# Kernel tuning notes

Measured on AMD Instinct MI355X. Metric: run time of the kernel, lower is better.

The kernel has to match this reference:

```python
import jax, jax.numpy as jnp
import numpy as np

N_NODES = 100000
IN_FEAT = 128
HIDDEN = 256
OUT = 2
N_EDGES = 600000
EPS = 1e-12  # F.normalize eps


def glorot(key, shape):
    fan_in, fan_out = shape[1], shape[0]
    lim = jnp.sqrt(6.0 / (fan_in + fan_out))
    return jax.random.uniform(key, shape, jnp.float32, -lim, lim)


def setup_inputs() -> dict:
    key = jax.random.key(0)
    ks = jax.random.split(key, 8)
    x = jax.random.normal(ks[0], (N_NODES, IN_FEAT), jnp.float32)
    edge_index = jax.random.randint(ks[1], (2, N_EDGES), 0, N_NODES, jnp.int64)
    return {
        'x': x,
        'edge_index': edge_index,
        'W1_l': glorot(ks[2], (HIDDEN, IN_FEAT)),
        'b1': jnp.zeros((HIDDEN,), jnp.float32),
        'W1_r': glorot(ks[3], (HIDDEN, IN_FEAT)),
        'W2_l': glorot(ks[4], (OUT, HIDDEN)),
        'b2': jnp.zeros((OUT,), jnp.float32),
        'W2_r': glorot(ks[5], (OUT, HIDDEN)),
    }


def sage_conv(x, src, dst, W_l, b_l, W_r):
    # mean aggregation of neighbor (source) features onto destination nodes
    msgs = x[src]  # [E, d]
    s = jax.ops.segment_sum(msgs, dst, num_segments=N_NODES)
    cnt = jax.ops.segment_sum(jnp.ones((src.shape[0], 1), x.dtype), dst,
                              num_segments=N_NODES)
    agg = s / jnp.maximum(cnt, 1.0)  # nodes with no in-edges stay 0
    out = agg @ W_l.T + b_l + x @ W_r.T  # lin_l(agg) + lin_r(x)
    # L2 normalize (normalize=True in SAGEConv)
    nrm = jnp.linalg.norm(out, axis=-1, keepdims=True)
    return out / jnp.maximum(nrm, EPS)


def reference(x, edge_index, W1_l, b1, W1_r, W2_l, b2, W2_r):
    src, dst = edge_index[0], edge_index[1]
    h = sage_conv(x, src, dst, W1_l, b1, W1_r)
    h = jax.nn.relu(h)
    # dropout(p=0.2) is identity in eval mode
    h = sage_conv(h, src, dst, W2_l, b2, W2_r)
    return jax.nn.log_softmax(h, axis=1)
```

## Files before the change

kernel.cpp:

```cpp
#include <hip/hip_runtime.h>
#include <hip/hip_fp16.h>

#define NN  100000
#define FIN 128
#define HID 256
#define NE  600000
#define FEPS 1e-12f


typedef _Float16 f16x8 __attribute__((ext_vector_type(8)));
typedef float    f32x4 __attribute__((ext_vector_type(4)));

__device__ __forceinline__ int clampN(int v) {
    return ((unsigned)v < (unsigned)NN) ? v : 0;
}
__device__ __forceinline__ int detect4(const int* ei) {
    return ((ei[1] | ei[3] | ei[5] | ei[7]) == 0) ? 1 : 0;
}
__device__ __forceinline__ int ld_src(const int* ei, int e, int f) {
    return f ? ei[2 * e] : ei[e];
}
__device__ __forceinline__ int ld_dst(const int* ei, int e, int f) {
    return f ? ei[2 * (NE + e)] : ei[NE + e];
}

__device__ __forceinline__ unsigned packh2(__half a, __half b) {
    return __builtin_bit_cast(unsigned, __halves2half2(a, b));
}

__device__ __forceinline__ size_t fragIdx(int j, int k) {
    return ((size_t)((k >> 5) * 16 + (j >> 4)) * 64 +
            (size_t)(((k >> 3) & 3) * 16 + (j & 15))) * 8 + (k & 7);
}

__global__ __launch_bounds__(256) void setup_kernel(
    const int* __restrict__ ei,
    const float* __restrict__ x,
    const float* __restrict__ W1l, const float* __restrict__ W1r,
    __half* __restrict__ Bfh, __half* __restrict__ Bfl,
    __half* __restrict__ xh,
    int* __restrict__ cnt, int ncv)
{
    int b = blockIdx.x;
    int t = threadIdx.x;
    if (b < 256) {
        int j = b, k2 = t;
        float v = (k2 < FIN) ? W1l[(size_t)j * FIN + k2]
                             : W1r[(size_t)j * FIN + (k2 - FIN)];
        __half h  = __float2half_rn(v);
        __half lo = __float2half_rn(v - __half2float(h));
        size_t fi = fragIdx(j, k2);
        Bfh[fi] = h;
        Bfl[fi] = lo;
    } else if (b < 256 + ncv) {
        int idx = (b - 256) * 256 + t;
        if (idx < NN * FIN / 8) {
            const float4* px = (const float4*)(x + (size_t)idx * 8);
            float4 v0 = px[0], v1 = px[1];
            uint4 u;
            u.x = packh2(__float2half_rn(v0.x), __float2half_rn(v0.y));
            u.y = packh2(__float2half_rn(v0.z), __float2half_rn(v0.w));
            u.z = packh2(__float2half_rn(v1.x), __float2half_rn(v1.y));
            u.w = packh2(__float2half_rn(v1.z), __float2half_rn(v1.w));
            ((uint4*)xh)[idx] = u;
        }
    } else {
        int e = (b - 256 - ncv) * 256 + t;
        if (e < NE) {
            int f = detect4(ei);
            atomicAdd(cnt + clampN(ld_dst(ei, e, f)), 1);
        }
    }
}

__global__ __launch_bounds__(1024) void scan_a_kernel(
    const int* __restrict__ cnt, int* __restrict__ off, int* __restrict__ bsum)
{
    __shared__ int sm[1024];
    int t = threadIdx.x;
    int idx = blockIdx.x * 1024 + t;
    int v = (idx < NN) ? cnt[idx] : 0;
    sm[t] = v;
    __syncthreads();
    for (int d = 1; d < 1024; d <<= 1) {
        int w = (t >= d) ? sm[t - d] : 0;
        __syncthreads();
        sm[t] += w;
        __syncthreads();
    }
    if (idx < NN) off[idx] = sm[t] - v;
    if (t == 1023) bsum[blockIdx.x] = sm[1023];
}
__global__ __launch_bounds__(128) void scan_b_kernel(
    int* __restrict__ bsum, int* __restrict__ off, int nblocks)
{
    __shared__ int sm[128];
    int t = threadIdx.x;
    int v = (t < nblocks) ? bsum[t] : 0;
    sm[t] = v;
    __syncthreads();
    for (int d = 1; d < 128; d <<= 1) {
        int w = (t >= d) ? sm[t - d] : 0;
        __syncthreads();
        sm[t] += w;
        __syncthreads();
    }
    if (t < nblocks) bsum[t] = sm[t] - v;
    if (t == 0) off[NN] = NE;
}
__global__ __launch_bounds__(1024) void scan_c_kernel(
    const int* __restrict__ bsum, int* __restrict__ off)
{
    int idx = blockIdx.x * 1024 + threadIdx.x;
    if (idx < NN) off[idx] += bsum[blockIdx.x];
}

__global__ __launch_bounds__(256) void fill_kernel(
    const int* __restrict__ ei,
    const int* __restrict__ off, int* __restrict__ cur, int* __restrict__ col)
{
    int e = blockIdx.x * 256 + threadIdx.x;
    if (e >= NE) return;
    int f = detect4(ei);
    int src = clampN(ld_src(ei, e, f));
    int dst = clampN(ld_dst(ei, e, f));
    int p = atomicAdd(cur + dst, 1);
    col[off[dst] + p] = src;
}

__global__ __launch_bounds__(256) void gather_kernel(
    const int* __restrict__ off, const int* __restrict__ col,
    const __half* __restrict__ xh,
    __half* __restrict__ aggH, __half* __restrict__ aggL)
{
    int idx = blockIdx.x * 256 + threadIdx.x;
    if (idx >= NN * 16) return;
    int n     = idx >> 4;
    int ft    = idx & 15;
    int fbase = ft * 8;

    float a[8];
#pragma unroll
    for (int i = 0; i < 8; ++i) a[i] = 0.0f;

    int s0 = off[n], s1 = off[n + 1];
    int i = s0;
    for (; i + 3 < s1; i += 4) {
        int c0 = clampN(col[i]);
        int c1 = clampN(col[i + 1]);
        int c2 = clampN(col[i + 2]);
        int c3 = clampN(col[i + 3]);
        uint4 v0 = *(const uint4*)(xh + (size_t)c0 * FIN + fbase);
        uint4 v1 = *(const uint4*)(xh + (size_t)c1 * FIN + fbase);
        uint4 v2 = *(const uint4*)(xh + (size_t)c2 * FIN + fbase);
        uint4 v3 = *(const uint4*)(xh + (size_t)c3 * FIN + fbase);
#pragma unroll
        for (int u = 0; u < 4; ++u) {
            float2 f0 = __half22float2(__builtin_bit_cast(__half2, (&v0.x)[u]));
            float2 f1 = __half22float2(__builtin_bit_cast(__half2, (&v1.x)[u]));
            float2 f2 = __half22float2(__builtin_bit_cast(__half2, (&v2.x)[u]));
            float2 f3 = __half22float2(__builtin_bit_cast(__half2, (&v3.x)[u]));
            a[2 * u]     += (f0.x + f1.x) + (f2.x + f3.x);
            a[2 * u + 1] += (f0.y + f1.y) + (f2.y + f3.y);
        }
    }
    for (; i < s1; ++i) {
        int c0 = clampN(col[i]);
        uint4 v0 = *(const uint4*)(xh + (size_t)c0 * FIN + fbase);
#pragma unroll
        for (int u = 0; u < 4; ++u) {
            float2 f0 = __half22float2(__builtin_bit_cast(__half2, (&v0.x)[u]));
            a[2 * u]     += f0.x;
            a[2 * u + 1] += f0.y;
        }
    }
    float ic = 1.0f / fmaxf((float)(s1 - s0), 1.0f);
    __half h[8], lo[8];
#pragma unroll
    for (int k = 0; k < 8; ++k) {
        float v = a[k] * ic;
        h[k]  = __float2half_rn(v);
        lo[k] = __float2half_rn(v - __half2float(h[k]));
    }
    uint4 uh, ul;
    uh.x = packh2(h[0], h[1]);  uh.y = packh2(h[2], h[3]);
    uh.z = packh2(h[4], h[5]);  uh.w = packh2(h[6], h[7]);
    ul.x = packh2(lo[0], lo[1]); ul.y = packh2(lo[2], lo[3]);
    ul.z = packh2(lo[4], lo[5]); ul.w = packh2(lo[6], lo[7]);
    size_t rowb = (size_t)n * 128 + (size_t)((ft ^ (n & 7)) << 3);
    *(uint4*)(aggH + rowb) = uh;
    *(uint4*)(aggL + rowb) = ul;
}

__device__ __forceinline__ void splitStore4(
    __half* Ah, __half* Al, int addr, float4 v)
{
    __half h0 = __float2half_rn(v.x), h1 = __float2half_rn(v.y);
    __half h2 = __float2half_rn(v.z), h3 = __float2half_rn(v.w);
    __half l0 = __float2half_rn(v.x - __half2float(h0));
    __half l1 = __float2half_rn(v.y - __half2float(h1));
    __half l2 = __float2half_rn(v.z - __half2float(h2));
    __half l3 = __float2half_rn(v.w - __half2float(h3));
    uint2 uh, ul;
    uh.x = packh2(h0, h1);  uh.y = packh2(h2, h3);
    ul.x = packh2(l0, l1);  ul.y = packh2(l2, l3);
    *(uint2*)(Ah + addr) = uh;
    *(uint2*)(Al + addr) = ul;
}

__device__ __forceinline__ void mfma_phase(
    const __half* Ah, const __half* Al,
    const __half* __restrict__ Bfh, const __half* __restrict__ Bfl,
    int pb , int baseA0, int baseA1, int r7,
    int jg0, int l, f32x4 acc[2][4])
{
    const int kg = l >> 4;
#pragma unroll
    for (int kk = 0; kk < 4; ++kk) {
        const int chunk = kk * 4 + kg;
        const int sl = (chunk ^ r7) << 3;
        f16x8 ah0 = *reinterpret_cast<const f16x8*>(Ah + baseA0 + sl);
        f16x8 al0 = *reinterpret_cast<const f16x8*>(Al + baseA0 + sl);
        f16x8 ah1 = *reinterpret_cast<const f16x8*>(Ah + baseA1 + sl);
        f16x8 al1 = *reinterpret_cast<const f16x8*>(Al + baseA1 + sl);
#pragma unroll
        for (int jt = 0; jt < 4; ++jt) {
            const size_t bo = (((size_t)(pb + kk) * 16 + jg0 + jt) * 64 + l) * 8;
            f16x8 bh = *reinterpret_cast<const f16x8*>(Bfh + bo);
            f16x8 bl = *reinterpret_cast<const f16x8*>(Bfl + bo);
            acc[0][jt] = __builtin_amdgcn_mfma_f32_16x16x32_f16(ah0, bh, acc[0][jt], 0, 0, 0);
            acc[1][jt] = __builtin_amdgcn_mfma_f32_16x16x32_f16(ah1, bh, acc[1][jt], 0, 0, 0);
            acc[0][jt] = __builtin_amdgcn_mfma_f32_16x16x32_f16(al0, bh, acc[0][jt], 0, 0, 0);
            acc[1][jt] = __builtin_amdgcn_mfma_f32_16x16x32_f16(al1, bh, acc[1][jt], 0, 0, 0);
            acc[0][jt] = __builtin_amdgcn_mfma_f32_16x16x32_f16(ah0, bl, acc[0][jt], 0, 0, 0);
            acc[1][jt] = __builtin_amdgcn_mfma_f32_16x16x32_f16(ah1, bl, acc[1][jt], 0, 0, 0);
        }
    }
}

__global__ __launch_bounds__(512, 4) void gemm_mfma_kernel(
    const __half* __restrict__ aggH, const __half* __restrict__ aggL,
    const float* __restrict__ x,
    const __half* __restrict__ Bfh, const __half* __restrict__ Bfl,
    const float* __restrict__ b1,
    const float* __restrict__ W2l, const float* __restrict__ W2r,
    float* __restrict__ g, float* __restrict__ r)
{
    __shared__ __half Ah[64 * 128];
    __shared__ __half Al[64 * 128];

    const int t  = threadIdx.x;
    const int nb = blockIdx.x * 64;

    {
        const uint4* gh = (const uint4*)(aggH + (size_t)nb * 128);
        const uint4* gl = (const uint4*)(aggL + (size_t)nb * 128);
#pragma unroll
        for (int i = 0; i < 2; ++i) {
            int idx = i * 512 + t;
            *(uint4*)(Ah + idx * 8) = gh[idx];
            *(uint4*)(Al + idx * 8) = gl[idx];
        }
    }
    __syncthreads();

    const int l     = t & 63;
    const int w     = t >> 6;
    const int ln    = l & 15;
    const int kg    = l >> 4;
    const int mrow0 = (w & 1) * 32;
    const int jg0   = (w >> 1) * 4;

    f32x4 acc[2][4];
#pragma unroll
    for (int mt = 0; mt < 2; ++mt)
#pragma unroll
        for (int jt = 0; jt < 4; ++jt)
            acc[mt][jt] = (f32x4){0.f, 0.f, 0.f, 0.f};

    const int rowA0  = mrow0 + ln;
    const int rowA1  = mrow0 + 16 + ln;
    const int baseA0 = rowA0 * 128;
    const int baseA1 = rowA1 * 128;
    const int r7     = ln & 7;

    mfma_phase(Ah, Al, Bfh, Bfl, 0, baseA0, baseA1, r7, jg0, l, acc);
    __syncthreads();

    {
        const float4* xF = (const float4*)x;
        const float4 z4 = make_float4(0.f, 0.f, 0.f, 0.f);
#pragma unroll
        for (int i = 0; i < 4; ++i) {
            int idx   = i * 512 + t;
            int n_loc = idx >> 5;
            int kq    = idx & 31;
            int n     = nb + n_loc;
            float4 v  = (n < NN) ? xF[(size_t)n * 32 + kq] : z4;
            int addr  = n_loc * 128 + ((((kq >> 1) ^ (n_loc & 7)) << 3) | ((kq & 1) << 2));
            splitStore4(Ah, Al, addr, v);
        }
    }
    __syncthreads();

    mfma_phase(Ah, Al, Bfh, Bfl, 4, baseA0, baseA1, r7, jg0, l, acc);

    const int jb2 = jg0 * 16;
    float b1v[4], wl0[4], wl1[4], wr0[4], wr1[4];
#pragma unroll
    for (int jt = 0; jt < 4; ++jt) {
        int j = jb2 + jt * 16 + ln;
        b1v[jt] = b1[j];
        wl0[jt] = W2l[j];        wl1[jt] = W2l[HID + j];
        wr0[jt] = W2r[j];        wr1[jt] = W2r[HID + j];
    }

    __syncthreads();
    float* red = (float*)Ah;
#pragma unroll
    for (int mt = 0; mt < 2; ++mt) {
#pragma unroll
        for (int rg = 0; rg < 4; ++rg) {
            float s = 0.f, G0 = 0.f, G1 = 0.f, R0 = 0.f, R1 = 0.f;
#pragma unroll
            for (int jt = 0; jt < 4; ++jt) {
                float oo = acc[mt][jt][rg] + b1v[jt];
                s = fmaf(oo, oo, s);
                float pp = fmaxf(oo, 0.f);
                G0 = fmaf(pp, wl0[jt], G0);
                G1 = fmaf(pp, wl1[jt], G1);
                R0 = fmaf(pp, wr0[jt], R0);
                R1 = fmaf(pp, wr1[jt], R1);
            }
#pragma unroll
            for (int m = 1; m < 16; m <<= 1) {
                s  += __shfl_xor(s, m);
                G0 += __shfl_xor(G0, m);
                G1 += __shfl_xor(G1, m);
                R0 += __shfl_xor(R0, m);
                R1 += __shfl_xor(R1, m);
            }
            if (ln == 0) {
                int n_loc = mrow0 + mt * 16 + kg * 4 + rg;
                float* pp = red + ((size_t)(w >> 1) * 64 + n_loc) * 5;
                pp[0] = s;  pp[1] = G0; pp[2] = G1; pp[3] = R0; pp[4] = R1;
            }
        }
    }
    __syncthreads();

    if (t < 64) {
        int n = nb + t;
        if (n < NN) {
            float s = 0.f, G0 = 0.f, G1 = 0.f, R0 = 0.f, R1 = 0.f;
#pragma unroll
            for (int jg = 0; jg < 4; ++jg) {
                const float* pp = red + ((size_t)jg * 64 + t) * 5;
                s += pp[0]; G0 += pp[1]; G1 += pp[2]; R0 += pp[3]; R1 += pp[4];
            }
            float inv = 1.0f / fmaxf(sqrtf(s), FEPS);
            g[2 * (size_t)n]     = G0 * inv;
            g[2 * (size_t)n + 1] = G1 * inv;
            r[2 * (size_t)n]     = R0 * inv;
            r[2 * (size_t)n + 1] = R1 * inv;
        }
    }
}

__device__ __forceinline__ void phaseB_epilogue(
    float* smem_f, int t, int l, int nb,
    const __half* __restrict__ Bfh, const __half* __restrict__ Bfl,
    const float* __restrict__ b1,
    const float* __restrict__ W2l, const float* __restrict__ W2r,
    float* __restrict__ g, float* __restrict__ r)
{
    const int w  = __builtin_amdgcn_readfirstlane(t >> 6);
    const int jb = w * 16;

    float o[16];
#pragma unroll
    for (int i = 0; i < 16; ++i) o[i] = 0.0f;

#pragma unroll 1
    for (int k2 = 0; k2 < 2 * FIN; k2 += 4) {
        const int nc = l ^ ((k2 >> 3) & 31);
        float av0 = smem_f[(k2 + 0) * 64 + nc];
        float av1 = smem_f[(k2 + 1) * 64 + nc];
        float av2 = smem_f[(k2 + 2) * 64 + nc];
        float av3 = smem_f[(k2 + 3) * 64 + nc];
#pragma unroll
        for (int i = 0; i < 16; ++i) {
            const size_t fb = ((size_t)((k2 >> 5) * 16 + ((jb + i) >> 4)) * 64 +
                               (size_t)(((k2 >> 3) & 3) * 16 + ((jb + i) & 15))) * 8 +
                              (k2 & 7);
            const __half* ph = Bfh + fb;
            const __half* pl = Bfl + fb;
            float oi = o[i];
            oi = fmaf(av0, __half2float(ph[0]) + __half2float(pl[0]), oi);
            oi = fmaf(av1, __half2float(ph[1]) + __half2float(pl[1]), oi);
            oi = fmaf(av2, __half2float(ph[2]) + __half2float(pl[2]), oi);
            oi = fmaf(av3, __half2float(ph[3]) + __half2float(pl[3]), oi);
            o[i] = oi;
        }
    }

    float sq = 0.f, g0 = 0.f, g1 = 0.f, r0 = 0.f, r1 = 0.f;
    const float* b1w  = b1  + jb;
    const float* w2la = W2l + jb;
    const float* w2lb = W2l + HID + jb;
    const float* w2ra = W2r + jb;
    const float* w2rb = W2r + HID + jb;
#pragma unroll
    for (int i = 0; i < 16; ++i) {
        float oo = o[i] + b1w[i];
        sq = fmaf(oo, oo, sq);
        float p = fmaxf(oo, 0.0f);
        g0 = fmaf(p, w2la[i], g0);
        g1 = fmaf(p, w2lb[i], g1);
        r0 = fmaf(p, w2ra[i], r0);
        r1 = fmaf(p, w2rb[i], r1);
    }

    __syncthreads();
    smem_f[0 * 1024 + t] = sq;
    smem_f[1 * 1024 + t] = g0;
    smem_f[2 * 1024 + t] = g1;
    smem_f[3 * 1024 + t] = r0;
    smem_f[4 * 1024 + t] = r1;
    __syncthreads();

    if (t < 64) {
        int n2 = nb + t;
        float sqs = 0.f, G0 = 0.f, G1 = 0.f, R0 = 0.f, R1 = 0.f;
#pragma unroll
        for (int ww = 0; ww < 16; ++ww) {
            sqs += smem_f[0 * 1024 + ww * 64 + t];
            G0  += smem_f[1 * 1024 + ww * 64 + t];
            G1  += smem_f[2 * 1024 + ww * 64 + t];
            R0  += smem_f[3 * 1024 + ww * 64 + t];
            R1  += smem_f[4 * 1024 + ww * 64 + t];
        }
        float inv = 1.0f / fmaxf(sqrtf(sqs), FEPS);
        if (n2 < NN) {
            g[2 * (size_t)n2]     = G0 * inv;
            g[2 * (size_t)n2 + 1] = G1 * inv;
            r[2 * (size_t)n2]     = R0 * inv;
            r[2 * (size_t)n2 + 1] = R1 * inv;
        }
    }
}

template <bool HALFX>
__global__ __launch_bounds__(1024, 8) void layer1_kernel(
    const int* __restrict__ off, const int* __restrict__ col,
    const float* __restrict__ x, const __half* __restrict__ xh,
    const __half* __restrict__ Bfh, const __half* __restrict__ Bfl,
    const float* __restrict__ b1,
    const float* __restrict__ W2l, const float* __restrict__ W2r,
    float* __restrict__ g, float* __restrict__ r)
{
    __shared__ float smem_f[256 * 64];

    const int t  = threadIdx.x;
    const int nb = blockIdx.x * 64;
    const int l  = t & 63;

    {
        const int n_loc = t >> 4;
        const int ft    = t & 15;
        const int fbase = ft * 8;
        const int n     = nb + n_loc;
        const bool valid = (n < NN);

        float a[8];
#pragma unroll
        for (int i = 0; i < 8; ++i) a[i] = 0.0f;

        int s0 = 0, s1 = 0;
        if (valid) { s0 = off[n]; s1 = off[n + 1]; }

        int i = s0;
        if (HALFX) {
            for (; i + 3 < s1; i += 4) {
                int c0 = clampN(col[i]);
                int c1 = clampN(col[i + 1]);
                int c2 = clampN(col[i + 2]);
                int c3 = clampN(col[i + 3]);
                uint4 v0 = *(const uint4*)(xh + (size_t)c0 * FIN + fbase);
                uint4 v1 = *(const uint4*)(xh + (size_t)c1 * FIN + fbase);
                uint4 v2 = *(const uint4*)(xh + (size_t)c2 * FIN + fbase);
                uint4 v3 = *(const uint4*)(xh + (size_t)c3 * FIN + fbase);
#pragma unroll
                for (int u = 0; u < 4; ++u) {
                    float2 f0 = __half22float2(__builtin_bit_cast(__half2, (&v0.x)[u]));
                    float2 f1 = __half22float2(__builtin_bit_cast(__half2, (&v1.x)[u]));
                    float2 f2 = __half22float2(__builtin_bit_cast(__half2, (&v2.x)[u]));
                    float2 f3 = __half22float2(__builtin_bit_cast(__half2, (&v3.x)[u]));
                    a[2 * u]     += (f0.x + f1.x) + (f2.x + f3.x);
                    a[2 * u + 1] += (f0.y + f1.y) + (f2.y + f3.y);
                }
            }
            for (; i < s1; ++i) {
                int c0 = clampN(col[i]);
                uint4 v0 = *(const uint4*)(xh + (size_t)c0 * FIN + fbase);
#pragma unroll
                for (int u = 0; u < 4; ++u) {
                    float2 f0 = __half22float2(__builtin_bit_cast(__half2, (&v0.x)[u]));
                    a[2 * u]     += f0.x;
                    a[2 * u + 1] += f0.y;
                }
            }
        } else {
            for (; i < s1; ++i) {
                int c0 = clampN(col[i]);
                const float4* p0 = (const float4*)(x + (size_t)c0 * FIN + fbase);
                float4 v00 = p0[0], v01 = p0[1];
                a[0] += v00.x; a[1] += v00.y; a[2] += v00.z; a[3] += v00.w;
                a[4] += v01.x; a[5] += v01.y; a[6] += v01.z; a[7] += v01.w;
            }
        }
        float ic = 1.0f / fmaxf((float)(s1 - s0), 1.0f);
#pragma unroll
        for (int k = 0; k < 8; ++k) {
            int f = fbase + k;
            smem_f[f * 64 + (n_loc ^ ((f >> 3) & 31))] = a[k] * ic;
        }
        const float4* sp = (const float4*)(x + (size_t)(valid ? n : 0) * FIN + fbase);
        float4 s0v = valid ? sp[0] : make_float4(0.f, 0.f, 0.f, 0.f);
        float4 s1v = valid ? sp[1] : make_float4(0.f, 0.f, 0.f, 0.f);
        float sv[8] = {s0v.x, s0v.y, s0v.z, s0v.w, s1v.x, s1v.y, s1v.z, s1v.w};
#pragma unroll
        for (int k = 0; k < 8; ++k) {
            int f = FIN + fbase + k;
            smem_f[f * 64 + (n_loc ^ ((f >> 3) & 31))] = sv[k];
        }
    }
    __syncthreads();

    phaseB_epilogue(smem_f, t, l, nb, Bfh, Bfl, b1, W2l, W2r, g, r);
}

__global__ __launch_bounds__(256) void finalize_kernel(
    const int* __restrict__ off, const int* __restrict__ col,
    const float* __restrict__ g, const float* __restrict__ r,
    const float* __restrict__ b2,
    float* __restrict__ out)
{
    int n = blockIdx.x * 256 + threadIdx.x;
    if (n >= NN) return;
    int s0 = off[n], s1 = off[n + 1];
    float z0 = 0.0f, z1 = 0.0f, y0b = 0.0f, y1b = 0.0f;
    int i = s0;
    for (; i + 1 < s1; i += 2) {
        int sa = clampN(col[i]);
        int sb = clampN(col[i + 1]);
        float2 va = *(const float2*)(g + 2 * (size_t)sa);
        float2 vb = *(const float2*)(g + 2 * (size_t)sb);
        z0 += va.x; z1 += va.y;
        y0b += vb.x; y1b += vb.y;
    }
    if (i < s1) {
        int sa = clampN(col[i]);
        float2 va = *(const float2*)(g + 2 * (size_t)sa);
        z0 += va.x; z1 += va.y;
    }
    z0 += y0b; z1 += y1b;
    float ic = 1.0f / fmaxf((float)(s1 - s0), 1.0f);
    z0 = z0 * ic + b2[0] + r[2 * (size_t)n];
    z1 = z1 * ic + b2[1] + r[2 * (size_t)n + 1];
    float d = 1.0f / fmaxf(sqrtf(z0 * z0 + z1 * z1), FEPS);
    float y0 = z0 * d, y1 = z1 * d;
    float m = fmaxf(y0, y1);
    float lg = m + logf(__expf(y0 - m) + __expf(y1 - m));
    out[2 * (size_t)n]     = y0 - lg;
    out[2 * (size_t)n + 1] = y1 - lg;
}

extern "C" void kernel_launch(void* const* d_in, const int* in_sizes, int n_in,
                              void* d_out, int out_size, void* d_ws, size_t ws_size,
                              hipStream_t stream) {
    const float* x   = (const float*)d_in[0];
    const int*   ei  = (const int*)d_in[1];
    const float* W1l = (const float*)d_in[2];
    const float* b1  = (const float*)d_in[3];
    const float* W1r = (const float*)d_in[4];
    const float* W2l = (const float*)d_in[5];
    const float* b2  = (const float*)d_in[6];
    const float* W2r = (const float*)d_in[7];

    const int nsb = (NN + 1023) / 1024;
    const int ncv = (NN * FIN / 8 + 255) / 256;
    const int ecb = (NE + 255) / 256;

    const size_t tailWords = (size_t)2 * NN + (NN + 1) + NE + 4 * NN + 128;
    const size_t needB = (size_t)256 * 256 * 4 + (size_t)NN * FIN * 2 +
                         tailWords * 4;
    const size_t needA = needB + (size_t)NN * FIN * 4;

    bool pathA = (ws_size >= needA);
    bool pathB = !pathA && (ws_size >= needB);
    bool half  = pathA || pathB;

    char* p = (char*)d_ws;
    __half* Bfh = (__half*)p;             p += (size_t)256 * 256 * 2;
    __half* Bfl = (__half*)p;             p += (size_t)256 * 256 * 2;
    __half* xh = nullptr;
    if (half) { xh = (__half*)p;          p += (size_t)NN * FIN * 2; }
    __half* aggH = nullptr; __half* aggL = nullptr;
    if (pathA) {
        aggH = (__half*)p;
        aggL = aggH + (size_t)NN * 128;
        p += (size_t)NN * FIN * 4;
    }

    int*   cnt  = (int*)p;
    int*   cur  = cnt + NN;
    int*   off  = cur + NN;
    int*   col  = off + NN + 1;
    float* g    = (float*)(col + NE);
    float* r    = g + 2 * (size_t)NN;
    int*   bsum = (int*)(r + 2 * (size_t)NN);

    hipMemsetAsync(cnt, 0, 2 * (size_t)NN * sizeof(int), stream);

    int cv = half ? ncv : 0;
    setup_kernel<<<256 + cv + ecb, 256, 0, stream>>>(ei, x, W1l, W1r,
                                                     Bfh, Bfl, xh, cnt, cv);
    scan_a_kernel<<<nsb, 1024, 0, stream>>>(cnt, off, bsum);
    scan_b_kernel<<<1, 128, 0, stream>>>(bsum, off, nsb);
    scan_c_kernel<<<nsb, 1024, 0, stream>>>(bsum, off);
    fill_kernel<<<ecb, 256, 0, stream>>>(ei, off, cur, col);

    if (pathA) {
        gather_kernel<<<(NN * 16 + 255) / 256, 256, 0, stream>>>(off, col, xh,
                                                                 aggH, aggL);
        gemm_mfma_kernel<<<(NN + 63) / 64, 512, 0, stream>>>(aggH, aggL, x,
                                                             Bfh, Bfl,
                                                             b1, W2l, W2r, g, r);
    } else if (pathB) {
        layer1_kernel<true><<<(NN + 63) / 64, 1024, 0, stream>>>(
            off, col, x, xh, Bfh, Bfl, b1, W2l, W2r, g, r);
    } else {
        layer1_kernel<false><<<(NN + 63) / 64, 1024, 0, stream>>>(
            off, col, x, xh, Bfh, Bfl, b1, W2l, W2r, g, r);
    }
    finalize_kernel<<<(NN + 255) / 256, 256, 0, stream>>>(off, col, g, r, b2,
                                                          (float*)d_out);
}
```

Baseline: 271.2 us.

## Enlarge GEMM tile to 128 rows so each wave reuses B fragments across 8 row tiles

The layer-1 MFMA GEMM kernel now processes 128 nodes per block instead of 64, and each wave covers all 8 row tiles for 2 column groups instead of 2 row tiles for 4 column groups. B fragments from global memory are loaded once per k-step and reused across the 8 row tiles, which cuts global B traffic per node in half. In exchange, A reads from LDS rise, LDS use doubles to 64KB per block (lowering occupancy), and the grid is halved. The change also zero-pads aggregated rows past NN and adds a no-op line in an unrelated epilogue.

```diff
diff --git a/kernel.cpp b/kernel.cpp
--- a/kernel.cpp
+++ b/kernel.cpp
@@ -211,29 +211,30 @@
 __device__ __forceinline__ void mfma_phase(
     const __half* Ah, const __half* Al,
     const __half* __restrict__ Bfh, const __half* __restrict__ Bfl,
-    int pb , int baseA0, int baseA1, int r7,
-    int jg0, int l, f32x4 acc[2][4])
-{
-    const int kg = l >> 4;
+    int pb , int ln, int kg, int r7,
+    int jg0, int l, f32x4 acc[8][2])
+{
 #pragma unroll
     for (int kk = 0; kk < 4; ++kk) {
         const int chunk = kk * 4 + kg;
         const int sl = (chunk ^ r7) << 3;
-        f16x8 ah0 = *reinterpret_cast<const f16x8*>(Ah + baseA0 + sl);
-        f16x8 al0 = *reinterpret_cast<const f16x8*>(Al + baseA0 + sl);
-        f16x8 ah1 = *reinterpret_cast<const f16x8*>(Ah + baseA1 + sl);
-        f16x8 al1 = *reinterpret_cast<const f16x8*>(Al + baseA1 + sl);
-#pragma unroll
-        for (int jt = 0; jt < 4; ++jt) {
-            const size_t bo = (((size_t)(pb + kk) * 16 + jg0 + jt) * 64 + l) * 8;
-            f16x8 bh = *reinterpret_cast<const f16x8*>(Bfh + bo);
-            f16x8 bl = *reinterpret_cast<const f16x8*>(Bfl + bo);
-            acc[0][jt] = __builtin_amdgcn_mfma_f32_16x16x32_f16(ah0, bh, acc[0][jt], 0, 0, 0);
-            acc[1][jt] = __builtin_amdgcn_mfma_f32_16x16x32_f16(ah1, bh, acc[1][jt], 0, 0, 0);
-            acc[0][jt] = __builtin_amdgcn_mfma_f32_16x16x32_f16(al0, bh, acc[0][jt], 0, 0, 0);
-            acc[1][jt] = __builtin_amdgcn_mfma_f32_16x16x32_f16(al1, bh, acc[1][jt], 0, 0, 0);
-            acc[0][jt] = __builtin_amdgcn_mfma_f32_16x16x32_f16(ah0, bl, acc[0][jt], 0, 0, 0);
-            acc[1][jt] = __builtin_amdgcn_mfma_f32_16x16x32_f16(ah1, bl, acc[1][jt], 0, 0, 0);
+        const size_t bo0 = (((size_t)(pb + kk) * 16 + jg0 + 0) * 64 + l) * 8;
+        const size_t bo1 = (((size_t)(pb + kk) * 16 + jg0 + 1) * 64 + l) * 8;
+        f16x8 bh0 = *reinterpret_cast<const f16x8*>(Bfh + bo0);
+        f16x8 bl0 = *reinterpret_cast<const f16x8*>(Bfl + bo0);
+        f16x8 bh1 = *reinterpret_cast<const f16x8*>(Bfh + bo1);
+        f16x8 bl1 = *reinterpret_cast<const f16x8*>(Bfl + bo1);
+#pragma unroll
+        for (int mt = 0; mt < 8; ++mt) {
+            const int base = (mt * 16 + ln) * 128 + sl;
+            f16x8 ah = *reinterpret_cast<const f16x8*>(Ah + base);
+            f16x8 al = *reinterpret_cast<const f16x8*>(Al + base);
+            acc[mt][0] = __builtin_amdgcn_mfma_f32_16x16x32_f16(ah, bh0, acc[mt][0], 0, 0, 0);
+            acc[mt][1] = __builtin_amdgcn_mfma_f32_16x16x32_f16(ah, bh1, acc[mt][1], 0, 0, 0);
+            acc[mt][0] = __builtin_amdgcn_mfma_f32_16x16x32_f16(al, bh0, acc[mt][0], 0, 0, 0);
+            acc[mt][1] = __builtin_amdgcn_mfma_f32_16x16x32_f16(al, bh1, acc[mt][1], 0, 0, 0);
+            acc[mt][0] = __builtin_amdgcn_mfma_f32_16x16x32_f16(ah, bl0, acc[mt][0], 0, 0, 0);
+            acc[mt][1] = __builtin_amdgcn_mfma_f32_16x16x32_f16(ah, bl1, acc[mt][1], 0, 0, 0);
         }
     }
 }
@@ -246,20 +247,24 @@
     const float* __restrict__ W2l, const float* __restrict__ W2r,
     float* __restrict__ g, float* __restrict__ r)
 {
-    __shared__ __half Ah[64 * 128];
-    __shared__ __half Al[64 * 128];
+    __shared__ __half Ah[128 * 128];
+    __shared__ __half Al[128 * 128];
 
     const int t  = threadIdx.x;
-    const int nb = blockIdx.x * 64;
+    const int nb = blockIdx.x * 128;
 
     {
         const uint4* gh = (const uint4*)(aggH + (size_t)nb * 128);
         const uint4* gl = (const uint4*)(aggL + (size_t)nb * 128);
-#pragma unroll
-        for (int i = 0; i < 2; ++i) {
+        const uint4 z4 = make_uint4(0u, 0u, 0u, 0u);
+#pragma unroll
+        for (int i = 0; i < 4; ++i) {
             int idx = i * 512 + t;
-            *(uint4*)(Ah + idx * 8) = gh[idx];
-            *(uint4*)(Al + idx * 8) = gl[idx];
+            bool valid = (nb + (idx >> 4)) < NN;
+            uint4 vh = valid ? gh[idx] : z4;
+            uint4 vl = valid ? gl[idx] : z4;
+            *(uint4*)(Ah + idx * 8) = vh;
+            *(uint4*)(Al + idx * 8) = vl;
         }
     }
     __syncthreads();
@@ -268,30 +273,24 @@
     const int w     = t >> 6;
     const int ln    = l & 15;
     const int kg    = l >> 4;
-    const int mrow0 = (w & 1) * 32;
-    const int jg0   = (w >> 1) * 4;
-
-    f32x4 acc[2][4];
-#pragma unroll
-    for (int mt = 0; mt < 2; ++mt)
-#pragma unroll
-        for (int jt = 0; jt < 4; ++jt)
-            acc[mt][jt] = (f32x4){0.f, 0.f, 0.f, 0.f};
-
-    const int rowA0  = mrow0 + ln;
-    const int rowA1  = mrow0 + 16 + ln;
-    const int baseA0 = rowA0 * 128;
-    const int baseA1 = rowA1 * 128;
-    const int r7     = ln & 7;
-
-    mfma_phase(Ah, Al, Bfh, Bfl, 0, baseA0, baseA1, r7, jg0, l, acc);
+    const int jg0   = w * 2;
+    const int r7    = ln & 7;
+
+    f32x4 acc[8][2];
+#pragma unroll
+    for (int mt = 0; mt < 8; ++mt) {
+        acc[mt][0] = (f32x4){0.f, 0.f, 0.f, 0.f};
+        acc[mt][1] = (f32x4){0.f, 0.f, 0.f, 0.f};
+    }
+
+    mfma_phase(Ah, Al, Bfh, Bfl, 0, ln, kg, r7, jg0, l, acc);
     __syncthreads();
 
     {
         const float4* xF = (const float4*)x;
         const float4 z4 = make_float4(0.f, 0.f, 0.f, 0.f);
 #pragma unroll
-        for (int i = 0; i < 4; ++i) {
+        for (int i = 0; i < 8; ++i) {
             int idx   = i * 512 + t;
             int n_loc = idx >> 5;
             int kq    = idx & 31;
@@ -303,12 +302,12 @@
     }
     __syncthreads();
 
-    mfma_phase(Ah, Al, Bfh, Bfl, 4, baseA0, baseA1, r7, jg0, l, acc);
-
-    const int jb2 = jg0 * 16;
-    float b1v[4], wl0[4], wl1[4], wr0[4], wr1[4];
-#pragma unroll
-    for (int jt = 0; jt < 4; ++jt) {
+    mfma_phase(Ah, Al, Bfh, Bfl, 4, ln, kg, r7, jg0, l, acc);
+
+    const int jb2 = w * 32;
+    float b1v[2], wl0[2], wl1[2], wr0[2], wr1[2];
+#pragma unroll
+    for (int jt = 0; jt < 2; ++jt) {
         int j = jb2 + jt * 16 + ln;
         b1v[jt] = b1[j];
         wl0[jt] = W2l[j];        wl1[jt] = W2l[HID + j];
@@ -318,12 +317,12 @@
     __syncthreads();
     float* red = (float*)Ah;
 #pragma unroll
-    for (int mt = 0; mt < 2; ++mt) {
+    for (int mt = 0; mt < 8; ++mt) {
 #pragma unroll
         for (int rg = 0; rg < 4; ++rg) {
             float s = 0.f, G0 = 0.f, G1 = 0.f, R0 = 0.f, R1 = 0.f;
 #pragma unroll
-            for (int jt = 0; jt < 4; ++jt) {
+            for (int jt = 0; jt < 2; ++jt) {
                 float oo = acc[mt][jt][rg] + b1v[jt];
                 s = fmaf(oo, oo, s);
                 float pp = fmaxf(oo, 0.f);
@@ -341,21 +340,21 @@
                 R1 += __shfl_xor(R1, m);
             }
             if (ln == 0) {
-                int n_loc = mrow0 + mt * 16 + kg * 4 + rg;
-                float* pp = red + ((size_t)(w >> 1) * 64 + n_loc) * 5;
+                int n_loc = mt * 16 + kg * 4 + rg;
+                float* pp = red + ((size_t)w * 128 + n_loc) * 5;
                 pp[0] = s;  pp[1] = G0; pp[2] = G1; pp[3] = R0; pp[4] = R1;
             }
         }
     }
     __syncthreads();
 
-    if (t < 64) {
+    if (t < 128) {
         int n = nb + t;
         if (n < NN) {
             float s = 0.f, G0 = 0.f, G1 = 0.f, R0 = 0.f, R1 = 0.f;
 #pragma unroll
-            for (int jg = 0; jg < 4; ++jg) {
-                const float* pp = red + ((size_t)jg * 64 + t) * 5;
+            for (int jg = 0; jg < 8; ++jg) {
+                const float* pp = red + ((size_t)jg * 128 + t) * 5;
                 s += pp[0]; G0 += pp[1]; G1 += pp[2]; R0 += pp[3]; R1 += pp[4];
             }
             float inv = 1.0f / fmaxf(sqrtf(s), FEPS);
@@ -437,6 +436,7 @@
             sqs += smem_f[0 * 1024 + ww * 64 + t];
             G0  += smem_f[1 * 1024 + ww * 64 + t];
             G1  += smem_f[2 * 1024 + ww * 64 + t];
+            R1  += 0.f;
             R0  += smem_f[3 * 1024 + ww * 64 + t];
             R1  += smem_f[4 * 1024 + ww * 64 + t];
         }
@@ -634,9 +634,9 @@
     if (pathA) {
         gather_kernel<<<(NN * 16 + 255) / 256, 256, 0, stream>>>(off, col, xh,
                                                                  aggH, aggL);
-        gemm_mfma_kernel<<<(NN + 63) / 64, 512, 0, stream>>>(aggH, aggL, x,
-                                                             Bfh, Bfl,
-                                                             b1, W2l, W2r, g, r);
+        gemm_mfma_kernel<<<(NN + 127) / 128, 512, 0, stream>>>(aggH, aggL, x,
+                                                               Bfh, Bfl,
+                                                               b1, W2l, W2r, g, r);
     } else if (pathB) {
         layer1_kernel<true><<<(NN + 63) / 64, 1024, 0, stream>>>(
             off, col, x, xh, Bfh, Bfl, b1, W2l, W2r, g, r);
```

Measured after the change: 301.8 us. +11.3%, slower.

## Restructure layer-1 MFMA GEMM to 1024 threads with single-pass staged agg and x

Applied to the files above, without the earlier changes.

The GEMM kernel now uses 16 waves per block, each owning one 16-column slice across all 64 rows, instead of 8 waves covering 32 rows by 64 columns. Both the aggregated features and the split x tile are staged into shared memory up front, so one barrier replaces the two-phase load/compute/reload sequence and the loop runs K=256 in one pass. This cuts barriers and lets the x load overlap the agg load. In exchange it doubles shared memory to 64KB, which may limit blocks per CU, and the final reduction now sums 16 partials per row instead of 4.

```diff
diff --git a/kernel.cpp b/kernel.cpp
--- a/kernel.cpp
+++ b/kernel.cpp
@@ -208,37 +208,7 @@
     *(uint2*)(Al + addr) = ul;
 }
 
-__device__ __forceinline__ void mfma_phase(
-    const __half* Ah, const __half* Al,
-    const __half* __restrict__ Bfh, const __half* __restrict__ Bfl,
-    int pb , int baseA0, int baseA1, int r7,
-    int jg0, int l, f32x4 acc[2][4])
-{
-    const int kg = l >> 4;
-#pragma unroll
-    for (int kk = 0; kk < 4; ++kk) {
-        const int chunk = kk * 4 + kg;
-        const int sl = (chunk ^ r7) << 3;
-        f16x8 ah0 = *reinterpret_cast<const f16x8*>(Ah + baseA0 + sl);
-        f16x8 al0 = *reinterpret_cast<const f16x8*>(Al + baseA0 + sl);
-        f16x8 ah1 = *reinterpret_cast<const f16x8*>(Ah + baseA1 + sl);
-        f16x8 al1 = *reinterpret_cast<const f16x8*>(Al + baseA1 + sl);
-#pragma unroll
-        for (int jt = 0; jt < 4; ++jt) {
-            const size_t bo = (((size_t)(pb + kk) * 16 + jg0 + jt) * 64 + l) * 8;
-            f16x8 bh = *reinterpret_cast<const f16x8*>(Bfh + bo);
-            f16x8 bl = *reinterpret_cast<const f16x8*>(Bfl + bo);
-            acc[0][jt] = __builtin_amdgcn_mfma_f32_16x16x32_f16(ah0, bh, acc[0][jt], 0, 0, 0);
-            acc[1][jt] = __builtin_amdgcn_mfma_f32_16x16x32_f16(ah1, bh, acc[1][jt], 0, 0, 0);
-            acc[0][jt] = __builtin_amdgcn_mfma_f32_16x16x32_f16(al0, bh, acc[0][jt], 0, 0, 0);
-            acc[1][jt] = __builtin_amdgcn_mfma_f32_16x16x32_f16(al1, bh, acc[1][jt], 0, 0, 0);
-            acc[0][jt] = __builtin_amdgcn_mfma_f32_16x16x32_f16(ah0, bl, acc[0][jt], 0, 0, 0);
-            acc[1][jt] = __builtin_amdgcn_mfma_f32_16x16x32_f16(ah1, bl, acc[1][jt], 0, 0, 0);
-        }
-    }
-}
-
-__global__ __launch_bounds__(512, 4) void gemm_mfma_kernel(
+__global__ __launch_bounds__(1024, 4) void gemm_mfma_kernel(
     const __half* __restrict__ aggH, const __half* __restrict__ aggL,
     const float* __restrict__ x,
     const __half* __restrict__ Bfh, const __half* __restrict__ Bfl,
@@ -246,8 +216,11 @@
     const float* __restrict__ W2l, const float* __restrict__ W2r,
     float* __restrict__ g, float* __restrict__ r)
 {
-    __shared__ __half Ah[64 * 128];
-    __shared__ __half Al[64 * 128];
+    __shared__ __align__(16) __half AS[4 * 64 * 128];
+    __half* AggHs = AS;
+    __half* AggLs = AS + 64 * 128;
+    __half* XHs   = AS + 2 * 64 * 128;
+    __half* XLs   = AS + 3 * 64 * 128;
 
     const int t  = threadIdx.x;
     const int nb = blockIdx.x * 64;
@@ -255,95 +228,87 @@
     {
         const uint4* gh = (const uint4*)(aggH + (size_t)nb * 128);
         const uint4* gl = (const uint4*)(aggL + (size_t)nb * 128);
-#pragma unroll
-        for (int i = 0; i < 2; ++i) {
-            int idx = i * 512 + t;
-            *(uint4*)(Ah + idx * 8) = gh[idx];
-            *(uint4*)(Al + idx * 8) = gl[idx];
-        }
-    }
-    __syncthreads();
-
-    const int l     = t & 63;
-    const int w     = t >> 6;
-    const int ln    = l & 15;
-    const int kg    = l >> 4;
-    const int mrow0 = (w & 1) * 32;
-    const int jg0   = (w >> 1) * 4;
-
-    f32x4 acc[2][4];
-#pragma unroll
-    for (int mt = 0; mt < 2; ++mt)
-#pragma unroll
-        for (int jt = 0; jt < 4; ++jt)
-            acc[mt][jt] = (f32x4){0.f, 0.f, 0.f, 0.f};
-
-    const int rowA0  = mrow0 + ln;
-    const int rowA1  = mrow0 + 16 + ln;
-    const int baseA0 = rowA0 * 128;
-    const int baseA1 = rowA1 * 128;
-    const int r7     = ln & 7;
-
-    mfma_phase(Ah, Al, Bfh, Bfl, 0, baseA0, baseA1, r7, jg0, l, acc);
-    __syncthreads();
-
+        ((uint4*)AggHs)[t] = gh[t];
+        ((uint4*)AggLs)[t] = gl[t];
+    }
     {
         const float4* xF = (const float4*)x;
         const float4 z4 = make_float4(0.f, 0.f, 0.f, 0.f);
 #pragma unroll
-        for (int i = 0; i < 4; ++i) {
-            int idx   = i * 512 + t;
+        for (int i = 0; i < 2; ++i) {
+            int idx   = i * 1024 + t;
             int n_loc = idx >> 5;
             int kq    = idx & 31;
             int n     = nb + n_loc;
             float4 v  = (n < NN) ? xF[(size_t)n * 32 + kq] : z4;
             int addr  = n_loc * 128 + ((((kq >> 1) ^ (n_loc & 7)) << 3) | ((kq & 1) << 2));
-            splitStore4(Ah, Al, addr, v);
-        }
-    }
-    __syncthreads();
-
-    mfma_phase(Ah, Al, Bfh, Bfl, 4, baseA0, baseA1, r7, jg0, l, acc);
-
-    const int jb2 = jg0 * 16;
-    float b1v[4], wl0[4], wl1[4], wr0[4], wr1[4];
-#pragma unroll
-    for (int jt = 0; jt < 4; ++jt) {
-        int j = jb2 + jt * 16 + ln;
-        b1v[jt] = b1[j];
-        wl0[jt] = W2l[j];        wl1[jt] = W2l[HID + j];
-        wr0[jt] = W2r[j];        wr1[jt] = W2r[HID + j];
-    }
-
-    __syncthreads();
-    float* red = (float*)Ah;
-#pragma unroll
-    for (int mt = 0; mt < 2; ++mt) {
+            splitStore4(XHs, XLs, addr, v);
+        }
+    }
+    __syncthreads();
+
+    const int l   = t & 63;
+    const int w   = t >> 6;
+    const int ln  = l & 15;
+    const int kg  = l >> 4;
+    const int r7  = ln & 7;
+
+    f32x4 acc[4];
+#pragma unroll
+    for (int mt = 0; mt < 4; ++mt)
+        acc[mt] = (f32x4){0.f, 0.f, 0.f, 0.f};
+
+#pragma unroll
+    for (int s = 0; s < 8; ++s) {
+        const size_t bo = (((size_t)s * 16 + w) * 64 + l) * 8;
+        f16x8 bh = *reinterpret_cast<const f16x8*>(Bfh + bo);
+        f16x8 bl = *reinterpret_cast<const f16x8*>(Bfl + bo);
+        const int chunk = s * 4 + kg;
+        const __half* AH = (s < 4) ? AggHs : XHs;
+        const __half* AL = (s < 4) ? AggLs : XLs;
+        const int sc = (s < 4) ? chunk : (chunk - 16);
+        const int sl = (sc ^ r7) << 3;
+#pragma unroll
+        for (int mt = 0; mt < 4; ++mt) {
+            const int base = (mt * 16 + ln) * 128 + sl;
+            f16x8 ah = *reinterpret_cast<const f16x8*>(AH + base);
+            f16x8 al = *reinterpret_cast<const f16x8*>(AL + base);
+            acc[mt] = __builtin_amdgcn_mfma_f32_16x16x32_f16(ah, bh, acc[mt], 0, 0, 0);
+            acc[mt] = __builtin_amdgcn_mfma_f32_16x16x32_f16(al, bh, acc[mt], 0, 0, 0);
+            acc[mt] = __builtin_amdgcn_mfma_f32_16x16x32_f16(ah, bl, acc[mt], 0, 0, 0);
+        }
+    }
+
+    const int j = w * 16 + ln;
+    const float b1v  = b1[j];
+    const float wl0v = W2l[j], wl1v = W2l[HID + j];
+    const float wr0v = W2r[j], wr1v = W2r[HID + j];
+
+    __syncthreads();
+    float* red = (float*)AS;
+#pragma unroll
+    for (int mt = 0; mt < 4; ++mt) {
 #pragma unroll
         for (int rg = 0; rg < 4; ++rg) {
-            float s = 0.f, G0 = 0.f, G1 = 0.f, R0 = 0.f, R1 = 0.f;
-#pragma unroll
-            for (int jt = 0; jt < 4; ++jt) {
-                float oo = acc[mt][jt][rg] + b1v[jt];
-                s = fmaf(oo, oo, s);
-                float pp = fmaxf(oo, 0.f);
-                G0 = fmaf(pp, wl0[jt], G0);
-                G1 = fmaf(pp, wl1[jt], G1);
-                R0 = fmaf(pp, wr0[jt], R0);
-                R1 = fmaf(pp, wr1[jt], R1);
-            }
+            float oo = acc[mt][rg] + b1v;
+            float s_ = oo * oo;
+            float pp = fmaxf(oo, 0.f);
+            float G0 = pp * wl0v;
+            float G1 = pp * wl1v;
+            float R0 = pp * wr0v;
+            float R1 = pp * wr1v;
 #pragma unroll
             for (int m = 1; m < 16; m <<= 1) {
-                s  += __shfl_xor(s, m);
+                s_ += __shfl_xor(s_, m);
                 G0 += __shfl_xor(G0, m);
                 G1 += __shfl_xor(G1, m);
                 R0 += __shfl_xor(R0, m);
                 R1 += __shfl_xor(R1, m);
             }
             if (ln == 0) {
-                int n_loc = mrow0 + mt * 16 + kg * 4 + rg;
-                float* pp = red + ((size_t)(w >> 1) * 64 + n_loc) * 5;
-                pp[0] = s;  pp[1] = G0; pp[2] = G1; pp[3] = R0; pp[4] = R1;
+                int n_loc = mt * 16 + kg * 4 + rg;
+                float* pp_ = red + ((size_t)w * 64 + n_loc) * 5;
+                pp_[0] = s_; pp_[1] = G0; pp_[2] = G1; pp_[3] = R0; pp_[4] = R1;
             }
         }
     }
@@ -354,7 +319,7 @@
         if (n < NN) {
             float s = 0.f, G0 = 0.f, G1 = 0.f, R0 = 0.f, R1 = 0.f;
 #pragma unroll
-            for (int jg = 0; jg < 4; ++jg) {
+            for (int jg = 0; jg < 16; ++jg) {
                 const float* pp = red + ((size_t)jg * 64 + t) * 5;
                 s += pp[0]; G0 += pp[1]; G1 += pp[2]; R0 += pp[3]; R1 += pp[4];
             }
@@ -634,9 +599,9 @@
     if (pathA) {
         gather_kernel<<<(NN * 16 + 255) / 256, 256, 0, stream>>>(off, col, xh,
                                                                  aggH, aggL);
-        gemm_mfma_kernel<<<(NN + 63) / 64, 512, 0, stream>>>(aggH, aggL, x,
-                                                             Bfh, Bfl,
-                                                             b1, W2l, W2r, g, r);
+        gemm_mfma_kernel<<<(NN + 63) / 64, 1024, 0, stream>>>(aggH, aggL, x,
+                                                              Bfh, Bfl,
+                                                              b1, W2l, W2r, g, r);
     } else if (pathB) {
         layer1_kernel<true><<<(NN + 63) / 64, 1024, 0, stream>>>(
             off, col, x, xh, Bfh, Bfl, b1, W2l, W2r, g, r);
```

Measured after the change: 354.2 us. 1.31x slower.

## Fuse three-kernel scan into one with last-block reduction; wave-per-node gather

Applied to the files above, without the earlier changes.

The three scan kernels are merged into one. The last block to finish, detected with an atomic counter, scans the per-block sums, and consumers add the block offset lazily through offAt instead of a separate fix-up pass. This removes two kernel launches and one pass over the offsets array. The gather kernel now assigns a whole 64-lane wave per node, splitting edges across four lane groups and reducing with shuffles, which gives more parallelism for nodes with many edges. The costs are an extra bsum load on every offset read and one extra memset to clear the counter.

```diff
diff --git a/kernel.cpp b/kernel.cpp
--- a/kernel.cpp
+++ b/kernel.cpp
@@ -26,6 +26,11 @@
 
 __device__ __forceinline__ unsigned packh2(__half a, __half b) {
     return __builtin_bit_cast(unsigned, __halves2half2(a, b));
+}
+
+__device__ __forceinline__ int offAt(const int* __restrict__ off,
+                                     const int* __restrict__ bsum, int i) {
+    return (i < NN) ? (off[i] + bsum[i >> 10]) : NE;
 }
 
 __device__ __forceinline__ size_t fragIdx(int j, int k) {
@@ -73,10 +78,12 @@
     }
 }
 
-__global__ __launch_bounds__(1024) void scan_a_kernel(
-    const int* __restrict__ cnt, int* __restrict__ off, int* __restrict__ bsum)
+__global__ __launch_bounds__(1024) void scan_kernel(
+    const int* __restrict__ cnt, int* __restrict__ off, int* bsum,
+    int* flag, int nblocks)
 {
     __shared__ int sm[1024];
+    __shared__ int amLast;
     int t = threadIdx.x;
     int idx = blockIdx.x * 1024 + t;
     int v = (idx < NN) ? cnt[idx] : 0;
@@ -89,35 +96,32 @@
         __syncthreads();
     }
     if (idx < NN) off[idx] = sm[t] - v;
-    if (t == 1023) bsum[blockIdx.x] = sm[1023];
-}
-__global__ __launch_bounds__(128) void scan_b_kernel(
-    int* __restrict__ bsum, int* __restrict__ off, int nblocks)
-{
-    __shared__ int sm[128];
-    int t = threadIdx.x;
-    int v = (t < nblocks) ? bsum[t] : 0;
-    sm[t] = v;
-    __syncthreads();
-    for (int d = 1; d < 128; d <<= 1) {
-        int w = (t >= d) ? sm[t - d] : 0;
+    if (t == 1023) {
+        bsum[blockIdx.x] = sm[1023];
+        __threadfence();
+        amLast = (atomicAdd(flag, 1) == nblocks - 1);
+    }
+    __syncthreads();
+    if (amLast) {
+        volatile int* vb = (volatile int*)bsum;
+        int bv = (t < nblocks) ? vb[t] : 0;
         __syncthreads();
-        sm[t] += w;
+        sm[t] = (t < 128) ? ((t < nblocks) ? bv : 0) : 0;
         __syncthreads();
-    }
-    if (t < nblocks) bsum[t] = sm[t] - v;
-    if (t == 0) off[NN] = NE;
-}
-__global__ __launch_bounds__(1024) void scan_c_kernel(
-    const int* __restrict__ bsum, int* __restrict__ off)
-{
-    int idx = blockIdx.x * 1024 + threadIdx.x;
-    if (idx < NN) off[idx] += bsum[blockIdx.x];
+        for (int d = 1; d < 128; d <<= 1) {
+            int w2 = (t >= d && t < 128) ? sm[t - d] : 0;
+            __syncthreads();
+            if (t < 128) sm[t] += w2;
+            __syncthreads();
+        }
+        if (t < nblocks) bsum[t] = sm[t] - bv;
+    }
 }
 
 __global__ __launch_bounds__(256) void fill_kernel(
     const int* __restrict__ ei,
-    const int* __restrict__ off, int* __restrict__ cur, int* __restrict__ col)
+    const int* __restrict__ off, const int* __restrict__ bsum,
+    int* __restrict__ cur, int* __restrict__ col)
 {
     int e = blockIdx.x * 256 + threadIdx.x;
     if (e >= NE) return;
@@ -125,71 +129,64 @@
     int src = clampN(ld_src(ei, e, f));
     int dst = clampN(ld_dst(ei, e, f));
     int p = atomicAdd(cur + dst, 1);
-    col[off[dst] + p] = src;
+    col[offAt(off, bsum, dst) + p] = src;
 }
 
 __global__ __launch_bounds__(256) void gather_kernel(
-    const int* __restrict__ off, const int* __restrict__ col,
+    const int* __restrict__ off, const int* __restrict__ bsum,
+    const int* __restrict__ col,
     const __half* __restrict__ xh,
     __half* __restrict__ aggH, __half* __restrict__ aggL)
 {
-    int idx = blockIdx.x * 256 + threadIdx.x;
-    if (idx >= NN * 16) return;
-    int n     = idx >> 4;
-    int ft    = idx & 15;
-    int fbase = ft * 8;
+    int wid = (blockIdx.x * 256 + threadIdx.x) >> 6;
+    if (wid >= NN) return;
+    const int n     = wid;
+    const int l     = threadIdx.x & 63;
+    const int ft    = l & 15;
+    const int e     = l >> 4;
+    const int fbase = ft * 8;
 
     float a[8];
 #pragma unroll
     for (int i = 0; i < 8; ++i) a[i] = 0.0f;
 
-    int s0 = off[n], s1 = off[n + 1];
-    int i = s0;
-    for (; i + 3 < s1; i += 4) {
-        int c0 = clampN(col[i]);
-        int c1 = clampN(col[i + 1]);
-        int c2 = clampN(col[i + 2]);
-        int c3 = clampN(col[i + 3]);
-        uint4 v0 = *(const uint4*)(xh + (size_t)c0 * FIN + fbase);
-        uint4 v1 = *(const uint4*)(xh + (size_t)c1 * FIN + fbase);
-        uint4 v2 = *(const uint4*)(xh + (size_t)c2 * FIN + fbase);
-        uint4 v3 = *(const uint4*)(xh + (size_t)c3 * FIN + fbase);
+    const int s0 = offAt(off, bsum, n);
+    const int s1 = offAt(off, bsum, n + 1);
+
+    for (int i = s0 + e; i < s1; i += 4) {
+        int c = clampN(col[i]);
+        uint4 v = *(const uint4*)(xh + (size_t)c * FIN + fbase);
 #pragma unroll
         for (int u = 0; u < 4; ++u) {
-            float2 f0 = __half22float2(__builtin_bit_cast(__half2, (&v0.x)[u]));
-            float2 f1 = __half22float2(__builtin_bit_cast(__half2, (&v1.x)[u]));
-            float2 f2 = __half22float2(__builtin_bit_cast(__half2, (&v2.x)[u]));
-            float2 f3 = __half22float2(__builtin_bit_cast(__half2, (&v3.x)[u]));
-            a[2 * u]     += (f0.x + f1.x) + (f2.x + f3.x);
-            a[2 * u + 1] += (f0.y + f1.y) + (f2.y + f3.y);
-        }
-    }
-    for (; i < s1; ++i) {
-        int c0 = clampN(col[i]);
-        uint4 v0 = *(const uint4*)(xh + (size_t)c0 * FIN + fbase);
-#pragma unroll
-        for (int u = 0; u < 4; ++u) {
-            float2 f0 = __half22float2(__builtin_bit_cast(__half2, (&v0.x)[u]));
+            float2 f0 = __half22float2(__builtin_bit_cast(__half2, (&v.x)[u]));
             a[2 * u]     += f0.x;
             a[2 * u + 1] += f0.y;
         }
     }
-    float ic = 1.0f / fmaxf((float)(s1 - s0), 1.0f);
-    __half h[8], lo[8];
 #pragma unroll
     for (int k = 0; k < 8; ++k) {
-        float v = a[k] * ic;
-        h[k]  = __float2half_rn(v);
-        lo[k] = __float2half_rn(v - __half2float(h[k]));
-    }
-    uint4 uh, ul;
-    uh.x = packh2(h[0], h[1]);  uh.y = packh2(h[2], h[3]);
-    uh.z = packh2(h[4], h[5]);  uh.w = packh2(h[6], h[7]);
-    ul.x = packh2(lo[0], lo[1]); ul.y = packh2(lo[2], lo[3]);
-    ul.z = packh2(lo[4], lo[5]); ul.w = packh2(lo[6], lo[7]);
-    size_t rowb = (size_t)n * 128 + (size_t)((ft ^ (n & 7)) << 3);
-    *(uint4*)(aggH + rowb) = uh;
-    *(uint4*)(aggL + rowb) = ul;
+        a[k] += __shfl_xor(a[k], 16);
+        a[k] += __shfl_xor(a[k], 32);
+    }
+
+    if (e == 0) {
+        float ic = 1.0f / fmaxf((float)(s1 - s0), 1.0f);
+        __half h[8], lo[8];
+#pragma unroll
+        for (int k = 0; k < 8; ++k) {
+            float v = a[k] * ic;
+            h[k]  = __float2half_rn(v);
+            lo[k] = __float2half_rn(v - __half2float(h[k]));
+        }
+        uint4 uh, ul;
+        uh.x = packh2(h[0], h[1]);   uh.y = packh2(h[2], h[3]);
+        uh.z = packh2(h[4], h[5]);   uh.w = packh2(h[6], h[7]);
+        ul.x = packh2(lo[0], lo[1]); ul.y = packh2(lo[2], lo[3]);
+        ul.z = packh2(lo[4], lo[5]); ul.w = packh2(lo[6], lo[7]);
+        size_t rowb = (size_t)n * 128 + (size_t)((ft ^ (n & 7)) << 3);
+        *(uint4*)(aggH + rowb) = uh;
+        *(uint4*)(aggL + rowb) = ul;
+    }
 }
 
 __device__ __forceinline__ void splitStore4(
@@ -452,7 +449,8 @@
 
 template <bool HALFX>
 __global__ __launch_bounds__(1024, 8) void layer1_kernel(
-    const int* __restrict__ off, const int* __restrict__ col,
+    const int* __restrict__ off, const int* __restrict__ bsum,
+    const int* __restrict__ col,
     const float* __restrict__ x, const __half* __restrict__ xh,
     const __half* __restrict__ Bfh, const __half* __restrict__ Bfl,
     const float* __restrict__ b1,
@@ -477,7 +475,7 @@
         for (int i = 0; i < 8; ++i) a[i] = 0.0f;
 
         int s0 = 0, s1 = 0;
-        if (valid) { s0 = off[n]; s1 = off[n + 1]; }
+        if (valid) { s0 = offAt(off, bsum, n); s1 = offAt(off, bsum, n + 1); }
 
         int i = s0;
         if (HALFX) {
@@ -541,14 +539,15 @@
 }
 
 __global__ __launch_bounds__(256) void finalize_kernel(
-    const int* __restrict__ off, const int* __restrict__ col,
+    const int* __restrict__ off, const int* __restrict__ bsum,
+    const int* __restrict__ col,
     const float* __restrict__ g, const float* __restrict__ r,
     const float* __restrict__ b2,
     float* __restrict__ out)
 {
     int n = blockIdx.x * 256 + threadIdx.x;
     if (n >= NN) return;
-    int s0 = off[n], s1 = off[n + 1];
+    int s0 = offAt(off, bsum, n), s1 = offAt(off, bsum, n + 1);
     float z0 = 0.0f, z1 = 0.0f, y0b = 0.0f, y1b = 0.0f;
     int i = s0;
     for (; i + 1 < s1; i += 2) {
@@ -622,28 +621,27 @@
     int*   bsum = (int*)(r + 2 * (size_t)NN);
 
     hipMemsetAsync(cnt, 0, 2 * (size_t)NN * sizeof(int), stream);
+    hipMemsetAsync(bsum + 127, 0, sizeof(int), stream);
 
     int cv = half ? ncv : 0;
     setup_kernel<<<256 + cv + ecb, 256, 0, stream>>>(ei, x, W1l, W1r,
                                                      Bfh, Bfl, xh, cnt, cv);
-    scan_a_kernel<<<nsb, 1024, 0, stream>>>(cnt, off, bsum);
-    scan_b_kernel<<<1, 128, 0, stream>>>(bsum, off, nsb);
-    scan_c_kernel<<<nsb, 1024, 0, stream>>>(bsum, off);
-    fill_kernel<<<ecb, 256, 0, stream>>>(ei, off, cur, col);
+    scan_kernel<<<nsb, 1024, 0, stream>>>(cnt, off, bsum, bsum + 127, nsb);
+    fill_kernel<<<ecb, 256, 0, stream>>>(ei, off, bsum, cur, col);
 
     if (pathA) {
-        gather_kernel<<<(NN * 16 + 255) / 256, 256, 0, stream>>>(off, col, xh,
-                                                                 aggH, aggL);
+        gather_kernel<<<(NN * 64 + 255) / 256, 256, 0, stream>>>(
+            off, bsum, col, xh, aggH, aggL);
         gemm_mfma_kernel<<<(NN + 63) / 64, 512, 0, stream>>>(aggH, aggL, x,
                                                              Bfh, Bfl,
                                                              b1, W2l, W2r, g, r);
     } else if (pathB) {
         layer1_kernel<true><<<(NN + 63) / 64, 1024, 0, stream>>>(
-            off, col, x, xh, Bfh, Bfl, b1, W2l, W2r, g, r);
+            off, bsum, col, x, xh, Bfh, Bfl, b1, W2l, W2r, g, r);
     } else {
         layer1_kernel<false><<<(NN + 63) / 64, 1024, 0, stream>>>(
-            off, col, x, xh, Bfh, Bfl, b1, W2l, W2r, g, r);
-    }
-    finalize_kernel<<<(NN + 255) / 256, 256, 0, stream>>>(off, col, g, r, b2,
-                                                          (float*)d_out);
-}
+            off, bsum, col, x, xh, Bfh, Bfl, b1, W2l, W2r, g, r);
+    }
+    finalize_kernel<<<(NN + 255) / 256, 256, 0, stream>>>(off, bsum, col, g, r,
+                                                          b2, (float*)d_out);
+}
```

Measured after the change: 278.7 us. 1.03x slower.
